# Optimization experiments

Measured on AMD Instinct MI355X. Metric: run time of the kernel, lower is better.

Reference implementation:

```python
import jax, jax.numpy as jnp
import numpy as np

B, T, I, H = 64, 2048, 256, 512


def setup_inputs() -> dict:
    key = jax.random.key(0)
    k1, k2, k3, k4, k5 = jax.random.split(key, 5)
    lim_ih = 1.0 / np.sqrt(H)
    return {
        "xs": jax.random.normal(k1, (B, T, I), dtype=jnp.float32),
        "w_ih": jax.random.uniform(k2, (3 * H, I), dtype=jnp.float32, minval=-lim_ih, maxval=lim_ih),
        "w_hh": jax.random.uniform(k3, (3 * H, H), dtype=jnp.float32, minval=-lim_ih, maxval=lim_ih),
        "b": jax.random.uniform(k4, (3 * H,), dtype=jnp.float32, minval=-lim_ih, maxval=lim_ih),
        "b_n": jax.random.uniform(k5, (H,), dtype=jnp.float32, minval=-lim_ih, maxval=lim_ih),
    }


def reference(xs, w_ih, w_hh, b, b_n):
    # xs: [B, T, I]. Equinox GRUCell gate order: (reset, update, new).
    hidden = w_hh.shape[1]

    def step(h, x):  # h: [B, H], x: [B, I]
        ig = x @ w_ih.T + b            # [B, 3H]
        hg = h @ w_hh.T                # [B, 3H]
        ir, iz, inew = jnp.split(ig, 3, axis=-1)
        hr, hz, hnew = jnp.split(hg, 3, axis=-1)
        r = jax.nn.sigmoid(ir + hr)
        z = jax.nn.sigmoid(iz + hz)
        n = jnp.tanh(inew + r * (hnew + b_n))
        h_new = n + z * (h - n)
        return h_new, None

    h0 = jnp.zeros((xs.shape[0], hidden), dtype=xs.dtype)
    xs_t = jnp.swapaxes(xs, 0, 1)  # [T, B, I] for scan over time
    h_final, _ = jax.lax.scan(step, h0, xs_t)
    return h_final  # [B, H]
```

## Files before the change

kernel.cpp:

```cpp
#include <hip/hip_runtime.h>
#include <stdint.h>

#define B_  64
#define T_  2048
#define I_  256
#define H_  512
#define NG  4
#define NP  8
#define HS  64

typedef __attribute__((ext_vector_type(8))) short  short8;
typedef __attribute__((ext_vector_type(4))) float  floatx4;
typedef __attribute__((ext_vector_type(4))) unsigned uintx4;
typedef unsigned long long u64;

#define CFLAGS_DW  2048
#define HPUB32_OFF 16384
#define XSB_OFF    (16384 + 2 * B_ * H_ * 4)
#define XSB_BYTES  ((size_t)T_ * NG * 8 * 1024)

__device__ __forceinline__ unsigned short f2bf(float f) {
    unsigned u = __float_as_uint(f);
    u = (u + 0x7fffu + ((u >> 16) & 1u)) >> 16;
    return (unsigned short)u;
}

__device__ __forceinline__ short8 ld8_bf(const float* p) {
    floatx4 a = *(const floatx4*)p;
    floatx4 c = *(const floatx4*)(p + 4);
    short8 r;
    r[0] = (short)f2bf(a[0]); r[1] = (short)f2bf(a[1]);
    r[2] = (short)f2bf(a[2]); r[3] = (short)f2bf(a[3]);
    r[4] = (short)f2bf(c[0]); r[5] = (short)f2bf(c[1]);
    r[6] = (short)f2bf(c[2]); r[7] = (short)f2bf(c[3]);
    return r;
}

__device__ __forceinline__ float sigf(float x) { return 1.f / (1.f + __expf(-x)); }
__device__ __forceinline__ float tanh_(float x) { return 2.f * sigf(2.f * x) - 1.f; }

__global__ __launch_bounds__(256, 1) void gru_persist(
    const float* __restrict__ xs, const float* __restrict__ w_ih,
    const float* __restrict__ w_hh, const float* __restrict__ b,
    const float* __restrict__ b_n, float* __restrict__ out,
    unsigned* __restrict__ flags, unsigned* __restrict__ hpub32,
    char* __restrict__ xsb, int use_xsb)
{
    const int tid  = threadIdx.x;
    const int wv   = tid >> 6;
    const int lane = tid & 63;
    const int q    = lane >> 4;
    const int c    = lane & 15;
    const int g    = blockIdx.x & (NG - 1);
    const int p    = blockIdx.x >> 2;
    const int hbase = p * HS + wv * 16;
    const int batch = g * 16 + c;

    __shared__ uintx4 smem[2][1280];

    short8 whh[3][16];
    short8 wih[3][8];
#pragma unroll
    for (int gate = 0; gate < 3; ++gate) {
        const float* wr = w_hh + (size_t)(gate * H_ + hbase + c) * H_ + q * 8;
#pragma unroll
        for (int kt = 0; kt < 16; ++kt) whh[gate][kt] = ld8_bf(wr + kt * 32);
        const float* wi = w_ih + (size_t)(gate * H_ + hbase + c) * I_ + q * 8;
#pragma unroll
        for (int kt = 0; kt < 8; ++kt)  wih[gate][kt] = ld8_bf(wi + kt * 32);
    }
    float br[4], bz[4], bni[4], bnn[4];
#pragma unroll
    for (int i = 0; i < 4; ++i) {
        int j = hbase + q * 4 + i;
        br[i]  = b[j];
        bz[i]  = b[H_ + j];
        bni[i] = b[2 * H_ + j];
        bnn[i] = b_n[j];
    }
    float hown[4] = {0.f, 0.f, 0.f, 0.f};

    if (use_xsb) {
        for (int k = 0; k < T_ / 32; ++k) {
            int t = k * 32 + p * 4 + wv;
            const float* src = xs + ((size_t)batch * T_ + t) * I_ + q * 8;
            char* db  = xsb + (((size_t)t * NG + g) << 13) + ((q * 16 + c) << 4);
            char* db2 = db + 4096;
            short8 v0 = ld8_bf(src + 0 * 32);
            short8 v1 = ld8_bf(src + 1 * 32);
            short8 v2 = ld8_bf(src + 2 * 32);
            short8 v3 = ld8_bf(src + 3 * 32);
            short8 v4 = ld8_bf(src + 4 * 32);
            short8 v5 = ld8_bf(src + 5 * 32);
            short8 v6 = ld8_bf(src + 6 * 32);
            short8 v7 = ld8_bf(src + 7 * 32);
            asm volatile("global_store_dwordx4 %0, %1, off sc0 sc1"             :: "v"(db),  "v"(v0) : "memory");
            asm volatile("global_store_dwordx4 %0, %1, off offset:1024 sc0 sc1" :: "v"(db),  "v"(v1) : "memory");
            asm volatile("global_store_dwordx4 %0, %1, off offset:2048 sc0 sc1" :: "v"(db),  "v"(v2) : "memory");
            asm volatile("global_store_dwordx4 %0, %1, off offset:3072 sc0 sc1" :: "v"(db),  "v"(v3) : "memory");
            asm volatile("global_store_dwordx4 %0, %1, off sc0 sc1"             :: "v"(db2), "v"(v4) : "memory");
            asm volatile("global_store_dwordx4 %0, %1, off offset:1024 sc0 sc1" :: "v"(db2), "v"(v5) : "memory");
            asm volatile("global_store_dwordx4 %0, %1, off offset:2048 sc0 sc1" :: "v"(db2), "v"(v6) : "memory");
            asm volatile("global_store_dwordx4 %0, %1, off offset:3072 sc0 sc1" :: "v"(db2), "v"(v7) : "memory");
        }
        asm volatile("s_waitcnt vmcnt(0)" ::: "memory");
        if (lane == 0) {
            unsigned one = 1;
            unsigned* cfa = flags + CFLAGS_DW + ((g * 32 + p * 4 + wv) << 4);
            asm volatile("global_store_dword %0, %1, off sc0 sc1" :: "v"(cfa), "v"(one) : "memory");
        }
        const unsigned* cfp = flags + CFLAGS_DW + ((g * 32 + (lane & 31)) << 4);
        for (;;) {
            unsigned cv;
            asm volatile("global_load_dword %0, %1, off sc0 sc1" : "=v"(cv) : "v"(cfp) : "memory");
            asm volatile("s_waitcnt vmcnt(0)" ::: "memory");
            if (__all(cv == 1u)) break;
            __builtin_amdgcn_s_sleep(1);
        }
    }

    short8 bx[8];
    if (use_xsb) {
        const char* xb  = xsb + (((size_t)0 * NG + g) << 13) + ((q * 16 + c) << 4);
        const char* xb2 = xb + 4096;
        asm volatile("global_load_dwordx4 %0, %1, off sc0 sc1"             : "=&v"(bx[0]) : "v"(xb)  : "memory");
        asm volatile("global_load_dwordx4 %0, %1, off offset:1024 sc0 sc1" : "=&v"(bx[1]) : "v"(xb)  : "memory");
        asm volatile("global_load_dwordx4 %0, %1, off offset:2048 sc0 sc1" : "=&v"(bx[2]) : "v"(xb)  : "memory");
        asm volatile("global_load_dwordx4 %0, %1, off offset:3072 sc0 sc1" : "=&v"(bx[3]) : "v"(xb)  : "memory");
        asm volatile("global_load_dwordx4 %0, %1, off sc0 sc1"             : "=&v"(bx[4]) : "v"(xb2) : "memory");
        asm volatile("global_load_dwordx4 %0, %1, off offset:1024 sc0 sc1" : "=&v"(bx[5]) : "v"(xb2) : "memory");
        asm volatile("global_load_dwordx4 %0, %1, off offset:2048 sc0 sc1" : "=&v"(bx[6]) : "v"(xb2) : "memory");
        asm volatile("global_load_dwordx4 %0, %1, off offset:3072 sc0 sc1" : "=&v"(bx[7]) : "v"(xb2) : "memory");
    }

    const unsigned* hq0 = hpub32 + (size_t)(g * 16 + c) * H_ + wv * 128 + q * 32;

    for (int t = 0; t < T_; ++t) {
        if (use_xsb) {
            asm volatile("s_waitcnt vmcnt(0)" ::: "memory");
            __builtin_amdgcn_sched_barrier(0);
        } else {
            const float* xrow = xs + ((size_t)batch * T_ + t) * I_ + q * 8;
#pragma unroll
            for (int kt = 0; kt < 8; ++kt) bx[kt] = ld8_bf(xrow + kt * 32);
        }

        floatx4 accr  = {br[0],  br[1],  br[2],  br[3]};
        floatx4 accz  = {bz[0],  bz[1],  bz[2],  bz[3]};
        floatx4 accni = {bni[0], bni[1], bni[2], bni[3]};
        floatx4 accnh = {0.f, 0.f, 0.f, 0.f};
#pragma unroll
        for (int kt = 0; kt < 8; ++kt) {
            accr  = __builtin_amdgcn_mfma_f32_16x16x32_bf16(wih[0][kt], bx[kt], accr,  0, 0, 0);
            accz  = __builtin_amdgcn_mfma_f32_16x16x32_bf16(wih[1][kt], bx[kt], accz,  0, 0, 0);
            accni = __builtin_amdgcn_mfma_f32_16x16x32_bf16(wih[2][kt], bx[kt], accni, 0, 0, 0);
        }
        __builtin_amdgcn_sched_barrier(0);

        const unsigned tcur = (unsigned)t;
        const unsigned* hb = hq0 + (size_t)(t & 1) * (B_ * H_);
        uintx4 st[8];
        for (;;) {
#pragma unroll
            for (int l = 0; l < 8; ++l)
                asm volatile("global_load_dwordx4 %0, %1, off offset:%2 sc0 sc1"
                             : "=&v"(st[l]) : "v"(hb), "n"(l * 16) : "memory");
            asm volatile("s_waitcnt vmcnt(0)" ::: "memory");
            __builtin_amdgcn_sched_barrier(0);
            unsigned chk = 0;
#pragma unroll
            for (int l = 0; l < 8; ++l) {
                chk |= st[l][0] ^ tcur; chk |= st[l][1] ^ tcur;
                chk |= st[l][2] ^ tcur; chk |= st[l][3] ^ tcur;
            }
            if (__all((chk & 0xffffu) == 0u)) break;
            __builtin_amdgcn_s_sleep(1);
        }

        char* sw   = (char*)smem + (t & 1) * 20480;
        char* srow = sw + (wv * 4 + q) * 1280 + c * 80;
#pragma unroll
        for (int w = 0; w < 4; ++w) {
            uintx4 pw;
            pw[0] = (st[2*w][0]   >> 16) | (st[2*w][1]   & 0xffff0000u);
            pw[1] = (st[2*w][2]   >> 16) | (st[2*w][3]   & 0xffff0000u);
            pw[2] = (st[2*w+1][0] >> 16) | (st[2*w+1][1] & 0xffff0000u);
            pw[3] = (st[2*w+1][2] >> 16) | (st[2*w+1][3] & 0xffff0000u);
            *(uintx4*)(srow + w * 16) = pw;
        }
        __syncthreads();

        const char* srd = sw + c * 80 + q * 16;
#pragma unroll
        for (int kt = 0; kt < 16; ++kt) {
            union { uintx4 u; short8 s; } bh;
            bh.u = *(const uintx4*)(srd + kt * 1280);
            accr  = __builtin_amdgcn_mfma_f32_16x16x32_bf16(whh[0][kt], bh.s, accr,  0, 0, 0);
            accz  = __builtin_amdgcn_mfma_f32_16x16x32_bf16(whh[1][kt], bh.s, accz,  0, 0, 0);
            accnh = __builtin_amdgcn_mfma_f32_16x16x32_bf16(whh[2][kt], bh.s, accnh, 0, 0, 0);
        }

#pragma unroll
        for (int i = 0; i < 4; ++i) {
            float r = sigf(accr[i]);
            float z = sigf(accz[i]);
            float n = tanh_(accni[i] + r * (accnh[i] + bnn[i]));
            hown[i] = n + z * (hown[i] - n);
        }

        if (t + 1 < T_) {
            unsigned tg = (unsigned)(t + 1);
            uintx4 pq;
            pq[0] = ((unsigned)f2bf(hown[0]) << 16) | tg;
            pq[1] = ((unsigned)f2bf(hown[1]) << 16) | tg;
            pq[2] = ((unsigned)f2bf(hown[2]) << 16) | tg;
            pq[3] = ((unsigned)f2bf(hown[3]) << 16) | tg;
            unsigned* dst = hpub32 + ((size_t)((t + 1) & 1) * B_ + g * 16 + c) * H_ + hbase + q * 4;
            asm volatile("global_store_dwordx4 %0, %1, off sc0 sc1" :: "v"(dst), "v"(pq) : "memory");

            if (use_xsb) {
                const char* xb  = xsb + (((size_t)(t + 1) * NG + g) << 13) + ((q * 16 + c) << 4);
                const char* xb2 = xb + 4096;
                asm volatile("global_load_dwordx4 %0, %1, off sc0 sc1"             : "=&v"(bx[0]) : "v"(xb)  : "memory");
                asm volatile("global_load_dwordx4 %0, %1, off offset:1024 sc0 sc1" : "=&v"(bx[1]) : "v"(xb)  : "memory");
                asm volatile("global_load_dwordx4 %0, %1, off offset:2048 sc0 sc1" : "=&v"(bx[2]) : "v"(xb)  : "memory");
                asm volatile("global_load_dwordx4 %0, %1, off offset:3072 sc0 sc1" : "=&v"(bx[3]) : "v"(xb)  : "memory");
                asm volatile("global_load_dwordx4 %0, %1, off sc0 sc1"             : "=&v"(bx[4]) : "v"(xb2) : "memory");
                asm volatile("global_load_dwordx4 %0, %1, off offset:1024 sc0 sc1" : "=&v"(bx[5]) : "v"(xb2) : "memory");
                asm volatile("global_load_dwordx4 %0, %1, off offset:2048 sc0 sc1" : "=&v"(bx[6]) : "v"(xb2) : "memory");
                asm volatile("global_load_dwordx4 %0, %1, off offset:3072 sc0 sc1" : "=&v"(bx[7]) : "v"(xb2) : "memory");
            }
        }
    }

    floatx4 o = {hown[0], hown[1], hown[2], hown[3]};
    *(floatx4*)(out + (size_t)batch * H_ + hbase + q * 4) = o;
}

extern "C" void kernel_launch(void* const* d_in, const int* in_sizes, int n_in,
                              void* d_out, int out_size, void* d_ws, size_t ws_size,
                              hipStream_t stream) {
    (void)in_sizes; (void)n_in; (void)out_size;
    const float* xs   = (const float*)d_in[0];
    const float* w_ih = (const float*)d_in[1];
    const float* w_hh = (const float*)d_in[2];
    const float* b    = (const float*)d_in[3];
    const float* b_n  = (const float*)d_in[4];
    float* out = (float*)d_out;

    unsigned* flags  = (unsigned*)d_ws;
    unsigned* hpub32 = (unsigned*)((char*)d_ws + HPUB32_OFF);
    char*     xsb    = (char*)d_ws + XSB_OFF;
    const int use_xsb = (ws_size >= (size_t)XSB_OFF + XSB_BYTES) ? 1 : 0;

    (void)hipMemsetAsync(d_ws, 0, XSB_OFF, stream);

    gru_persist<<<NG * NP, 256, 0, stream>>>(xs, w_ih, w_hh, b, b_n, out,
                                             flags, hpub32, xsb, use_xsb);
}
```

Before: 7.455 ms.

## Speculatively poll hidden state with sc0-only loads and prefetch x after sync

The hidden-state poll is now issued before the input-projection MFMAs, so its latency overlaps that compute. Polls use loads with only the sc0 cache hint, which may hit a nearer cache level, and fall back to sc0 sc1 loads after a bounded number of failed rounds. The fast path is disabled for good if a fallback load succeeds where the fast ones did not. The next step's x prefetch moves to just after the sync completes. The risk is reading stale cached values, which costs extra spin rounds or forces permanent fallback, and the change adds cross-step coherence subtleties.

Result: slower. 7.951 ms (+6.7%).

```diff
diff --git a/kernel.cpp b/kernel.cpp
--- a/kernel.cpp
+++ b/kernel.cpp
@@ -8,6 +8,7 @@
 #define NG  4
 #define NP  8
 #define HS  64
+#define FAST_ROUNDS 6
 
 typedef __attribute__((ext_vector_type(8))) short  short8;
 typedef __attribute__((ext_vector_type(4))) float  floatx4;
@@ -38,6 +39,30 @@
 
 __device__ __forceinline__ float sigf(float x) { return 1.f / (1.f + __expf(-x)); }
 __device__ __forceinline__ float tanh_(float x) { return 2.f * sigf(2.f * x) - 1.f; }
+
+__device__ __forceinline__ void poll_issue(uintx4 (&st)[8], const unsigned* hb, bool fast) {
+    if (fast) {
+#pragma unroll
+        for (int l = 0; l < 8; ++l)
+            asm volatile("global_load_dwordx4 %0, %1, off offset:%2 sc0"
+                         : "=&v"(st[l]) : "v"(hb), "n"(l * 16) : "memory");
+    } else {
+#pragma unroll
+        for (int l = 0; l < 8; ++l)
+            asm volatile("global_load_dwordx4 %0, %1, off offset:%2 sc0 sc1"
+                         : "=&v"(st[l]) : "v"(hb), "n"(l * 16) : "memory");
+    }
+}
+
+__device__ __forceinline__ bool poll_check(const uintx4 (&st)[8], unsigned tcur) {
+    unsigned chk = 0;
+#pragma unroll
+    for (int l = 0; l < 8; ++l) {
+        chk |= st[l][0] ^ tcur; chk |= st[l][1] ^ tcur;
+        chk |= st[l][2] ^ tcur; chk |= st[l][3] ^ tcur;
+    }
+    return __all((chk & 0xffffu) == 0u) != 0;
+}
 
 __global__ __launch_bounds__(256, 1) void gru_persist(
     const float* __restrict__ xs, const float* __restrict__ w_ih,
@@ -135,15 +160,22 @@
 
     const unsigned* hq0 = hpub32 + (size_t)(g * 16 + c) * H_ + wv * 128 + q * 32;
 
+    bool nofast = false;
+
     for (int t = 0; t < T_; ++t) {
-        if (use_xsb) {
-            asm volatile("s_waitcnt vmcnt(0)" ::: "memory");
-            __builtin_amdgcn_sched_barrier(0);
-        } else {
+        const unsigned tcur = (unsigned)t;
+        const unsigned* hb = hq0 + (size_t)(t & 1) * (B_ * H_);
+        const bool fast_elig = (!nofast) && (t >= 8);
+        uintx4 st[8];
+
+        if (!use_xsb) {
             const float* xrow = xs + ((size_t)batch * T_ + t) * I_ + q * 8;
 #pragma unroll
             for (int kt = 0; kt < 8; ++kt) bx[kt] = ld8_bf(xrow + kt * 32);
         }
+        poll_issue(st, hb, fast_elig);
+        asm volatile("s_waitcnt vmcnt(0)" ::: "memory");
+        __builtin_amdgcn_sched_barrier(0);
 
         floatx4 accr  = {br[0],  br[1],  br[2],  br[3]};
         floatx4 accz  = {bz[0],  bz[1],  bz[2],  bz[3]};
@@ -157,24 +189,34 @@
         }
         __builtin_amdgcn_sched_barrier(0);
 
-        const unsigned tcur = (unsigned)t;
-        const unsigned* hb = hq0 + (size_t)(t & 1) * (B_ * H_);
-        uintx4 st[8];
-        for (;;) {
-#pragma unroll
-            for (int l = 0; l < 8; ++l)
-                asm volatile("global_load_dwordx4 %0, %1, off offset:%2 sc0 sc1"
-                             : "=&v"(st[l]) : "v"(hb), "n"(l * 16) : "memory");
-            asm volatile("s_waitcnt vmcnt(0)" ::: "memory");
-            __builtin_amdgcn_sched_barrier(0);
-            unsigned chk = 0;
-#pragma unroll
-            for (int l = 0; l < 8; ++l) {
-                chk |= st[l][0] ^ tcur; chk |= st[l][1] ^ tcur;
-                chk |= st[l][2] ^ tcur; chk |= st[l][3] ^ tcur;
+        if (!poll_check(st, tcur)) {
+            int  fr = fast_elig ? (FAST_ROUNDS - 1) : 0;
+            bool slow_failed = false;
+            for (;;) {
+                const bool uf = (fr > 0);
+                poll_issue(st, hb, uf);
+                asm volatile("s_waitcnt vmcnt(0)" ::: "memory");
+                __builtin_amdgcn_sched_barrier(0);
+                if (poll_check(st, tcur)) {
+                    if (fast_elig && !uf && !slow_failed) nofast = true;
+                    break;
+                }
+                if (uf) --fr; else slow_failed = true;
+                __builtin_amdgcn_s_sleep(1);
             }
-            if (__all((chk & 0xffffu) == 0u)) break;
-            __builtin_amdgcn_s_sleep(1);
+        }
+
+        if (use_xsb && t + 1 < T_) {
+            const char* xb  = xsb + (((size_t)(t + 1) * NG + g) << 13) + ((q * 16 + c) << 4);
+            const char* xb2 = xb + 4096;
+            asm volatile("global_load_dwordx4 %0, %1, off sc0 sc1"             : "=&v"(bx[0]) : "v"(xb)  : "memory");
+            asm volatile("global_load_dwordx4 %0, %1, off offset:1024 sc0 sc1" : "=&v"(bx[1]) : "v"(xb)  : "memory");
+            asm volatile("global_load_dwordx4 %0, %1, off offset:2048 sc0 sc1" : "=&v"(bx[2]) : "v"(xb)  : "memory");
+            asm volatile("global_load_dwordx4 %0, %1, off offset:3072 sc0 sc1" : "=&v"(bx[3]) : "v"(xb)  : "memory");
+            asm volatile("global_load_dwordx4 %0, %1, off sc0 sc1"             : "=&v"(bx[4]) : "v"(xb2) : "memory");
+            asm volatile("global_load_dwordx4 %0, %1, off offset:1024 sc0 sc1" : "=&v"(bx[5]) : "v"(xb2) : "memory");
+            asm volatile("global_load_dwordx4 %0, %1, off offset:2048 sc0 sc1" : "=&v"(bx[6]) : "v"(xb2) : "memory");
+            asm volatile("global_load_dwordx4 %0, %1, off offset:3072 sc0 sc1" : "=&v"(bx[7]) : "v"(xb2) : "memory");
         }
 
         char* sw   = (char*)smem + (t & 1) * 20480;
@@ -217,19 +259,6 @@
             pq[3] = ((unsigned)f2bf(hown[3]) << 16) | tg;
             unsigned* dst = hpub32 + ((size_t)((t + 1) & 1) * B_ + g * 16 + c) * H_ + hbase + q * 4;
             asm volatile("global_store_dwordx4 %0, %1, off sc0 sc1" :: "v"(dst), "v"(pq) : "memory");
-
-            if (use_xsb) {
-                const char* xb  = xsb + (((size_t)(t + 1) * NG + g) << 13) + ((q * 16 + c) << 4);
-                const char* xb2 = xb + 4096;
-                asm volatile("global_load_dwordx4 %0, %1, off sc0 sc1"             : "=&v"(bx[0]) : "v"(xb)  : "memory");
-                asm volatile("global_load_dwordx4 %0, %1, off offset:1024 sc0 sc1" : "=&v"(bx[1]) : "v"(xb)  : "memory");
-                asm volatile("global_load_dwordx4 %0, %1, off offset:2048 sc0 sc1" : "=&v"(bx[2]) : "v"(xb)  : "memory");
-                asm volatile("global_load_dwordx4 %0, %1, off offset:3072 sc0 sc1" : "=&v"(bx[3]) : "v"(xb)  : "memory");
-                asm volatile("global_load_dwordx4 %0, %1, off sc0 sc1"             : "=&v"(bx[4]) : "v"(xb2) : "memory");
-                asm volatile("global_load_dwordx4 %0, %1, off offset:1024 sc0 sc1" : "=&v"(bx[5]) : "v"(xb2) : "memory");
-                asm volatile("global_load_dwordx4 %0, %1, off offset:2048 sc0 sc1" : "=&v"(bx[6]) : "v"(xb2) : "memory");
-                asm volatile("global_load_dwordx4 %0, %1, off offset:3072 sc0 sc1" : "=&v"(bx[7]) : "v"(xb2) : "memory");
-            }
         }
     }
 
```
